# Kernel optimization log

Measured on AMD Instinct MI355X. Metric: run time of the kernel, lower is better.

The kernel has to match this reference:

```python
import jax, jax.numpy as jnp
import numpy as np


def _scinol_new_p(p0, S2, G, eta, M, cond):
    # SCINOL effective-parameter computation (done under no_grad in torch)
    denom = jnp.sqrt(S2 + M * M)
    theta = jnp.clip(G / denom, -1.0, 1.0)
    upd = jnp.where(cond, theta / (2.0 * denom) * eta, 0.0)
    return p0 + jax.lax.stop_gradient(upd)


def _conv(x, w, b):
    y = jax.lax.conv_general_dilated(x, w, window_strides=(1, 1), padding='VALID',
                                     dimension_numbers=('NCHW', 'OIHW', 'NCHW'))
    return y + b[None, :, None, None]


def _maxpool2(x):
    return jax.lax.reduce_window(x, -jnp.inf, jax.lax.max, (1, 1, 2, 2), (1, 1, 2, 2), 'VALID')


def _scinol_conv(x, w0, wS2, wG, weta, wM, b0, bS2, bG, beta):
    # M-update: per-input-channel mean (over batch) of max-abs over H,W
    stat = jax.lax.stop_gradient(jnp.mean(jnp.max(jnp.abs(x), axis=(2, 3)), axis=0))  # (C_in,)
    M = jnp.maximum(stat, wM)  # (C_in,)
    w = _scinol_new_p(w0, wS2, wG, weta, M[None, :, None, None], wG != 0)
    b = _scinol_new_p(b0, bS2, bG, beta, jnp.float32(1.0), bG != 0)
    return _conv(x, w, b)


def _scinol_linear(x, w0, wS2, wG, weta, wM, b0, bS2, bG, beta):
    stat = jax.lax.stop_gradient(jnp.mean(jnp.abs(x), axis=0))  # (in_features,)
    M = jnp.maximum(wM, stat)  # broadcast -> (out, in)
    w = _scinol_new_p(w0, wS2, wG, weta, M, wS2 != 0)
    b = _scinol_new_p(b0, bS2, bG, beta, jnp.float32(1.0), bS2 != 0)
    return x @ w.T + b


def setup_inputs() -> dict:
    key = jax.random.key(0)
    ks = iter(jax.random.split(key, 40))
    f32 = jnp.float32
    d = {}
    d['x'] = jax.random.normal(next(ks), (2048, 1, 28, 28), dtype=f32)
    for pre, wshape, cin in [('c1', (64, 1, 5, 5), 1), ('c2', (64, 64, 5, 5), 64)]:
        d[pre + '_w0'] = jax.random.normal(next(ks), wshape, dtype=f32) * 0.1
        d[pre + '_wS2'] = jax.random.uniform(next(ks), wshape, dtype=f32)
        d[pre + '_wG'] = jax.random.normal(next(ks), wshape, dtype=f32)
        d[pre + '_weta'] = jax.random.uniform(next(ks), wshape, dtype=f32)
        d[pre + '_wM'] = jax.random.uniform(next(ks), (cin,), dtype=f32)
        d[pre + '_b0'] = jax.random.normal(next(ks), (64,), dtype=f32) * 0.1
        d[pre + '_bS2'] = jax.random.uniform(next(ks), (64,), dtype=f32)
        d[pre + '_bG'] = jax.random.normal(next(ks), (64,), dtype=f32)
        d[pre + '_beta'] = jax.random.uniform(next(ks), (64,), dtype=f32)
    d['l_w0'] = jax.random.normal(next(ks), (10, 1024), dtype=f32) * 0.03
    d['l_wS2'] = jax.random.uniform(next(ks), (10, 1024), dtype=f32)
    d['l_wG'] = jax.random.normal(next(ks), (10, 1024), dtype=f32)
    d['l_weta'] = jax.random.uniform(next(ks), (10, 1024), dtype=f32)
    d['l_wM'] = jax.random.uniform(next(ks), (10, 1024), dtype=f32)
    d['l_b0'] = jax.random.normal(next(ks), (10,), dtype=f32) * 0.03
    d['l_bS2'] = jax.random.uniform(next(ks), (10,), dtype=f32)
    d['l_bG'] = jax.random.normal(next(ks), (10,), dtype=f32)
    d['l_beta'] = jax.random.uniform(next(ks), (10,), dtype=f32)
    return d


def reference(x,
              c1_w0, c1_wS2, c1_wG, c1_weta, c1_wM, c1_b0, c1_bS2, c1_bG, c1_beta,
              c2_w0, c2_wS2, c2_wG, c2_weta, c2_wM, c2_b0, c2_bS2, c2_bG, c2_beta,
              l_w0, l_wS2, l_wG, l_weta, l_wM, l_b0, l_bS2, l_bG, l_beta):
    h = _scinol_conv(x, c1_w0, c1_wS2, c1_wG, c1_weta, c1_wM, c1_b0, c1_bS2, c1_bG, c1_beta)
    h = _maxpool2(jax.nn.relu(h))                      # (N,64,12,12)
    h = _scinol_conv(h, c2_w0, c2_wS2, c2_wG, c2_weta, c2_wM, c2_b0, c2_bS2, c2_bG, c2_beta)
    h = _maxpool2(jax.nn.relu(h))                      # (N,64,4,4)
    h = h.reshape(h.shape[0], -1)                      # (N,1024)
    return _scinol_linear(h, l_w0, l_wS2, l_wG, l_weta, l_wM, l_b0, l_bS2, l_bG, l_beta)
```

## Files before the change

### kernel.cpp

```cpp
#include <hip/hip_runtime.h>
#include <hip/hip_bf16.h>

typedef float v4f __attribute__((ext_vector_type(4)));
typedef short v8s __attribute__((ext_vector_type(8)));

#define WS_STAT2   0
#define WS_STATL   64
#define WS_B1      1088
#define WS_B2      1152
#define WS_WL      1216
#define WS_BL      11456
#define WS_IMAX    11520
#define WS_W1F_B   54272
#define WS_WP2_B   62464
#define WS_P1_B    267264
#define WS_P2_B    38016000
#define WS_C1MAX_F 9504000
#define WS_LPART_F 66816

__global__ void k_stat1(const float* __restrict__ x, float* ws) {
    int tid = threadIdx.x;
    int wv = tid >> 6, lane = tid & 63;
    int n = blockIdx.x * 4 + wv;
    const float* p = x + n * 784;
    float m = 0.f;
    for (int i = lane; i < 784; i += 64) m = fmaxf(m, fabsf(p[i]));
#pragma unroll
    for (int off = 32; off; off >>= 1) m = fmaxf(m, __shfl_xor(m, off, 64));
    if (lane == 0) ws[WS_IMAX + n] = m;
}

__global__ void k_prepw1(const float* __restrict__ w0, const float* __restrict__ S2,
                         const float* __restrict__ G, const float* __restrict__ eta,
                         const float* __restrict__ wM,
                         const float* __restrict__ b0, const float* __restrict__ bS2,
                         const float* __restrict__ bG, const float* __restrict__ beta,
                         float* ws) {
    __shared__ float red[256];
    int tid = threadIdx.x;
    float p = 0.f;
    for (int i = tid; i < 2048; i += 256) p += ws[WS_IMAX + i];
    red[tid] = p;
    __syncthreads();
    for (int s = 128; s > 0; s >>= 1) {
        if (tid < s) red[tid] += red[tid + s];
        __syncthreads();
    }
    float M = fmaxf(red[0] * (1.f / 2048.f), wM[0]);

    int i = blockIdx.x * 256 + tid;
    if (i < 4096) {
        int j = i & 7, m16 = (i >> 3) & 15, q = (i >> 7) & 3, ot = i >> 9;
        int tap = q * 8 + j, oc = m16 * 4 + ot;
        float v = 0.f;
        if (tap < 25) {
            int s = oc * 25 + tap;
            float g = G[s];
            float den = sqrtf(S2[s] + M * M);
            float inv = 1.f / den;
            float th = fminf(fmaxf(g * inv, -1.f), 1.f);
            v = w0[s] + ((g != 0.f) ? th * 0.5f * inv * eta[s] : 0.f);
        }
        ((__hip_bfloat16*)((char*)ws + WS_W1F_B))[i] = __float2bfloat16(v);
    } else if (i < 4160) {
        int c = i - 4096;
        float g = bG[c];
        float den = sqrtf(bS2[c] + 1.f);
        float inv = 1.f / den;
        float th = fminf(fmaxf(g * inv, -1.f), 1.f);
        ws[WS_B1 + c] = b0[c] + ((g != 0.f) ? th * 0.5f * inv * beta[c] : 0.f);
    }
}

__global__ void __launch_bounds__(256)
k_conv1(const float* __restrict__ x, float* ws, __hip_bfloat16* __restrict__ pool1) {
    __shared__ __align__(16) float sX[1024];
    __shared__ int sMax[64];
    int n = blockIdx.x, tid = threadIdx.x;
    int wv = tid >> 6, lane = tid & 63;
    int m16 = lane & 15, quad = lane >> 4;

    {
        const float4* src = (const float4*)(x + (size_t)n * 784);
        float4 v = {0.f, 0.f, 0.f, 0.f};
        if (tid < 196) v = src[tid];
        ((float4*)sX)[tid] = v;
    }
    if (tid < 64) sMax[tid] = 0;

    const ushort* wfrag = (const ushort*)((const char*)ws + WS_W1F_B);
    v8s bfr[4];
#pragma unroll
    for (int ot = 0; ot < 4; ++ot)
        bfr[ot] = *(const v8s*)(wfrag + ((ot * 4 + quad) * 16 + m16) * 8);
    float4 bias = *(const float4*)(ws + WS_B1 + m16 * 4);

    int dj[8];
#pragma unroll
    for (int j = 0; j < 8; ++j) {
        int tap = quad * 8 + j;
        int u = (tap * 13) >> 6;
        dj[j] = tap + 23 * u;
    }

    int W0 = wv * 36 + (m16 >> 2);
    int wy = (W0 * 171) >> 11;
    int wx = W0 - wy * 12;
    int coff = 28 * ((m16 >> 1) & 1) + (m16 & 1);

    __syncthreads();

    float vmax[4] = {0.f, 0.f, 0.f, 0.f};
    ushort* op = (ushort*)(pool1 + (size_t)n * 9216);

    float g[8];
    {
        int base = 56 * wy + 2 * wx + coff;
#pragma unroll
        for (int j = 0; j < 8; ++j) g[j] = sX[base + dj[j]];
    }
    for (int mt = 0; mt < 9; ++mt) {
        union { v8s v; ushort us[8]; } ua;
#pragma unroll
        for (int j = 0; j < 8; ++j)
            ua.us[j] = __bfloat16_as_ushort(__float2bfloat16(g[j]));

        wx += 4;
        if (wx >= 12) { wx -= 12; ++wy; }
        if (mt < 8) {
            int nb = 56 * wy + 2 * wx + coff;
#pragma unroll
            for (int j = 0; j < 8; ++j) g[j] = sX[nb + dj[j]];
        }

        v4f z = {0.f, 0.f, 0.f, 0.f};
        v4f acc[4];
#pragma unroll
        for (int ot = 0; ot < 4; ++ot)
            acc[ot] = __builtin_amdgcn_mfma_f32_16x16x32_bf16(ua.v, bfr[ot], z, 0, 0, 0);

        int Wd = (wv * 9 + mt) * 4 + quad;
        ushort4 pk;
#pragma unroll
        for (int ot = 0; ot < 4; ++ot) {
            v4f a = acc[ot];
            float m = fmaxf(fmaxf(a[0], a[1]), fmaxf(a[2], a[3]));
            float pv = fmaxf(m + bias[ot], 0.f);
            vmax[ot] = fmaxf(vmax[ot], pv);
            ((ushort*)&pk)[ot] = __bfloat16_as_ushort(__float2bfloat16(pv));
        }
        *(ushort4*)(op + Wd * 64 + m16 * 4) = pk;
    }

#pragma unroll
    for (int ot = 0; ot < 4; ++ot) {
        float m = vmax[ot];
        m = fmaxf(m, __shfl_xor(m, 16, 64));
        m = fmaxf(m, __shfl_xor(m, 32, 64));
        if (lane < 16) atomicMax(&sMax[lane * 4 + ot], __float_as_int(m));
    }
    __syncthreads();
    if (tid < 64) ws[WS_C1MAX_F + n * 64 + tid] = __int_as_float(sMax[tid]);
}

__global__ void k_stat2red(float* ws) {
    __shared__ float red[256];
    int c = blockIdx.x, t = threadIdx.x;
    float s = 0.f;
    for (int n = t; n < 2048; n += 256) s += ws[WS_C1MAX_F + n * 64 + c];
    red[t] = s;
    __syncthreads();
    for (int k = 128; k > 0; k >>= 1) {
        if (t < k) red[t] += red[t + k];
        __syncthreads();
    }
    if (t == 0) ws[WS_STAT2 + c] = red[0] * (1.f / 2048.f);
}

__global__ void k_prepw2(const float* __restrict__ w0, const float* __restrict__ S2,
                         const float* __restrict__ G, const float* __restrict__ eta,
                         const float* __restrict__ wM,
                         const float* __restrict__ b0, const float* __restrict__ bS2,
                         const float* __restrict__ bG, const float* __restrict__ beta,
                         float* ws, __hip_bfloat16* __restrict__ wp2) {
    int i = blockIdx.x * 256 + threadIdx.x;
    int j = i & 7, m16 = (i >> 3) & 15, quad = (i >> 7) & 3;
    int ot = (i >> 9) & 3, kc = (i >> 11) & 1, uv = i >> 12;
    int oc = ot * 16 + m16, ic = kc * 32 + quad * 8 + j;
    int s = oc * 1600 + ic * 25 + uv;
    float M = fmaxf(ws[WS_STAT2 + ic], wM[ic]);
    float g = G[s];
    float den = sqrtf(S2[s] + M * M);
    float inv = 1.f / den;
    float th = fminf(fmaxf(g * inv, -1.f), 1.f);
    float v = w0[s] + ((g != 0.f) ? th * 0.5f * inv * eta[s] : 0.f);
    wp2[i] = __float2bfloat16(v);
    if (blockIdx.x == 0 && threadIdx.x < 64) {
        int c = threadIdx.x;
        float gb = bG[c];
        float den2 = sqrtf(bS2[c] + 1.f);
        float inv2 = 1.f / den2;
        float th2 = fminf(fmaxf(gb * inv2, -1.f), 1.f);
        ws[WS_B2 + c] = b0[c] + ((gb != 0.f) ? th2 * 0.5f * inv2 * beta[c] : 0.f);
    }
}

#define LOADB(buf, uvi) do {                                                   \
    const ushort* wnext_ = wlane + (uvi) * 4096;                               \
    _Pragma("unroll")                                                          \
    for (int kc_ = 0; kc_ < 2; ++kc_)                                          \
        _Pragma("unroll")                                                      \
        for (int ot_ = 0; ot_ < 4; ++ot_)                                      \
            buf[kc_ * 4 + ot_] = *(const v8s*)(wnext_ + (kc_ * 4 + ot_) * 512);\
} while (0)

#define STEP(buf, uvi) do {                                                    \
    int u_ = (uvi) / 5, v_ = (uvi) % 5;                                        \
    int r0_ = rbase + u_ * 12 + v_;                                            \
    _Pragma("unroll")                                                          \
    for (int kc_ = 0; kc_ < 2; ++kc_) {                                        \
        v8s pA_[4];                                                            \
        _Pragma("unroll")                                                      \
        for (int pt_ = 0; pt_ < 4; ++pt_) {                                    \
            int row_ = r0_ + pt_ * 24;                                         \
            int rs_ = row_ & 7;                                                \
            pA_[pt_] = *(const v8s*)(simg + row_ * 64 +                        \
                                     (((kc_ * 4 + quad) ^ rs_) << 3));         \
        }                                                                      \
        _Pragma("unroll")                                                      \
        for (int pt_ = 0; pt_ < 4; ++pt_)                                      \
            _Pragma("unroll")                                                  \
            for (int ot_ = 0; ot_ < 4; ++ot_)                                  \
                acc[pt_][ot_] = __builtin_amdgcn_mfma_f32_16x16x32_bf16(       \
                    pA_[pt_], buf[kc_ * 4 + ot_], acc[pt_][ot_], 0, 0, 0);     \
    }                                                                          \
} while (0)

__global__ void __launch_bounds__(256, 2)
k_conv2(const ushort* __restrict__ pool1, const ushort* __restrict__ wp2,
        const float* __restrict__ ws, float* __restrict__ pool2) {
    __shared__ __align__(16) ushort sImg[4 * 9216];
    int tid = threadIdx.x;
    int wv = tid >> 6, lane = tid & 63;
    int n0 = blockIdx.x * 4;

    {
        const uint4* src = (const uint4*)(pool1 + (size_t)n0 * 9216);
        uint4* dst = (uint4*)sImg;
#pragma unroll
        for (int img = 0; img < 4; ++img) {
            int b = img * 1152;
#pragma unroll
            for (int i = 0; i < 4; ++i) {
                int c = tid + i * 256;
                int r = c >> 3, col = c & 7;
                dst[b + r * 8 + (col ^ (r & 7))] = src[b + c];
            }
            if (tid < 128) {
                int c = 1024 + tid;
                int r = c >> 3, col = c & 7;
                dst[b + r * 8 + (col ^ (r & 7))] = src[b + c];
            }
        }
    }

    int m16 = lane & 15, quad = lane >> 4;
    int x0 = m16 & 7;
    int yb = m16 >> 3;
    int rbase = yb * 12 + x0;

    v4f acc[4][4];
#pragma unroll
    for (int i = 0; i < 4; ++i)
#pragma unroll
        for (int j = 0; j < 4; ++j) acc[i][j] = (v4f){0.f, 0.f, 0.f, 0.f};

    const ushort* wlane = wp2 + lane * 8;

    v8s b0[8], b1[8];
    LOADB(b0, 0);

    __syncthreads();

    const ushort* simg = sImg + wv * 9216;

#pragma unroll
    for (int t = 0; t < 12; ++t) {
        LOADB(b1, 2 * t + 1);
        STEP(b0, 2 * t);
        LOADB(b0, 2 * t + 2);
        STEP(b1, 2 * t + 1);
    }
    STEP(b0, 24);

    int n = n0 + wv;
    float bv[4];
#pragma unroll
    for (int ot = 0; ot < 4; ++ot) bv[ot] = ws[WS_B2 + ot * 16 + m16];
    float* outp = pool2 + (size_t)n * 1024;
#pragma unroll
    for (int pt = 0; pt < 4; ++pt)
#pragma unroll
        for (int ot = 0; ot < 4; ++ot) {
            v4f a = acc[pt][ot];
            float m01 = fmaxf(a[0], a[1]);
            float m23 = fmaxf(a[2], a[3]);
            m01 = fmaxf(m01, __shfl_xor(m01, 32, 64));
            m23 = fmaxf(m23, __shfl_xor(m23, 32, 64));
            if (lane < 32) {
                int oc = ot * 16 + m16;
                int f = oc * 16 + pt * 4 + (quad & 1) * 2;
                outp[f] = fmaxf(m01 + bv[ot], 0.f);
                outp[f + 1] = fmaxf(m23 + bv[ot], 0.f);
            }
        }
}

__global__ void k_statl(const float* __restrict__ pool2, float* ws) {
    int b = blockIdx.x, tid = threadIdx.x;
    float4 s = {0.f, 0.f, 0.f, 0.f};
    for (int im = 0; im < 32; ++im) {
        float4 v = ((const float4*)(pool2 + (size_t)(b * 32 + im) * 1024))[tid];
        s.x += v.x; s.y += v.y; s.z += v.z; s.w += v.w;
    }
    ((float4*)(ws + WS_LPART_F + b * 1024))[tid] = s;
}

__global__ void k_prepwl(const float* __restrict__ w0, const float* __restrict__ S2,
                         const float* __restrict__ G, const float* __restrict__ eta,
                         const float* __restrict__ wM,
                         const float* __restrict__ b0, const float* __restrict__ bS2,
                         const float* __restrict__ bG, const float* __restrict__ beta,
                         float* ws) {
    int i = blockIdx.x * 256 + threadIdx.x;
    if (i < 10240) {
        int f = i & 1023;
        float s = 0.f;
#pragma unroll
        for (int b = 0; b < 64; ++b) s += ws[WS_LPART_F + b * 1024 + f];
        float stat = s * (1.f / 2048.f);
        float M = fmaxf(wM[i], stat);
        float s2 = S2[i];
        float den = sqrtf(s2 + M * M);
        float inv = 1.f / den;
        float th = fminf(fmaxf(G[i] * inv, -1.f), 1.f);
        ws[WS_WL + i] = w0[i] + ((s2 != 0.f) ? th * 0.5f * inv * eta[i] : 0.f);
    } else if (i < 10250) {
        int c = i - 10240;
        float s2 = bS2[c];
        float den = sqrtf(s2 + 1.f);
        float inv = 1.f / den;
        float th = fminf(fmaxf(bG[c] * inv, -1.f), 1.f);
        ws[WS_BL + c] = b0[c] + ((s2 != 0.f) ? th * 0.5f * inv * beta[c] : 0.f);
    }
}

__global__ void k_linear(const float* __restrict__ pool2, const float* __restrict__ ws,
                         float* __restrict__ out) {
    int tid = threadIdx.x;
    int wv = tid >> 6, lane = tid & 63;
    int n = blockIdx.x * 4 + wv;
    const float* hp = pool2 + (size_t)n * 1024;
    float h[16];
#pragma unroll
    for (int j = 0; j < 16; ++j) h[j] = hp[j * 64 + lane];
    for (int oc = 0; oc < 10; ++oc) {
        const float* wp = ws + WS_WL + oc * 1024;
        float d = 0.f;
#pragma unroll
        for (int j = 0; j < 16; ++j) d = fmaf(h[j], wp[j * 64 + lane], d);
#pragma unroll
        for (int off = 32; off; off >>= 1) d += __shfl_xor(d, off, 64);
        if (lane == 0) out[n * 10 + oc] = d + ws[WS_BL + oc];
    }
}

extern "C" void kernel_launch(void* const* d_in, const int* in_sizes, int n_in,
                              void* d_out, int out_size, void* d_ws, size_t ws_size,
                              hipStream_t stream) {
    const float* x = (const float*)d_in[0];
    float* ws = (float*)d_ws;
    __hip_bfloat16* wp2 = (__hip_bfloat16*)((char*)d_ws + WS_WP2_B);
    __hip_bfloat16* p1 = (__hip_bfloat16*)((char*)d_ws + WS_P1_B);
    float* p2 = (float*)((char*)d_ws + WS_P2_B);
    float* out = (float*)d_out;

    k_stat1<<<512, 256, 0, stream>>>(x, ws);
    k_prepw1<<<17, 256, 0, stream>>>(
        (const float*)d_in[1], (const float*)d_in[2], (const float*)d_in[3],
        (const float*)d_in[4], (const float*)d_in[5], (const float*)d_in[6],
        (const float*)d_in[7], (const float*)d_in[8], (const float*)d_in[9], ws);
    k_conv1<<<2048, 256, 0, stream>>>(x, ws, p1);
    k_stat2red<<<64, 256, 0, stream>>>(ws);
    k_prepw2<<<400, 256, 0, stream>>>(
        (const float*)d_in[10], (const float*)d_in[11], (const float*)d_in[12],
        (const float*)d_in[13], (const float*)d_in[14], (const float*)d_in[15],
        (const float*)d_in[16], (const float*)d_in[17], (const float*)d_in[18], ws, wp2);
    k_conv2<<<512, 256, 0, stream>>>((const ushort*)p1, (const ushort*)wp2, ws, p2);
    k_statl<<<64, 256, 0, stream>>>(p2, ws);
    k_prepwl<<<41, 256, 0, stream>>>(
        (const float*)d_in[19], (const float*)d_in[20], (const float*)d_in[21],
        (const float*)d_in[22], (const float*)d_in[23], (const float*)d_in[24],
        (const float*)d_in[25], (const float*)d_in[26], (const float*)d_in[27], ws);
    k_linear<<<512, 256, 0, stream>>>(p2, ws, out);
}
```

Baseline: 200.9 us.

## Stage conv2 weights through LDS with double-buffered A fragments

In conv2, each wave used to fetch weight fragments straight from global memory. Now the block cooperatively loads each weight slice into a shared LDS buffer, prefetches the next slices into registers, and separates the steps with barriers. Image fragments are double-buffered in registers so the next tap loads while the current MFMAs run. Conv1 now converts its input tile to bf16 once when filling LDS rather than on every use. The linear-layer statistic reduction uses twice as many blocks. The conv2 change cuts redundant global weight traffic but adds block-wide barriers and brings LDS use close to the per-CU limit at two blocks per CU.

After: 196.1 us. -2.4%, faster.

```diff
diff --git a/kernel.cpp b/kernel.cpp
--- a/kernel.cpp
+++ b/kernel.cpp
@@ -74,7 +74,7 @@
 
 __global__ void __launch_bounds__(256)
 k_conv1(const float* __restrict__ x, float* ws, __hip_bfloat16* __restrict__ pool1) {
-    __shared__ __align__(16) float sX[1024];
+    __shared__ __align__(16) ushort sXh[1024];
     __shared__ int sMax[64];
     int n = blockIdx.x, tid = threadIdx.x;
     int wv = tid >> 6, lane = tid & 63;
@@ -84,7 +84,12 @@
         const float4* src = (const float4*)(x + (size_t)n * 784);
         float4 v = {0.f, 0.f, 0.f, 0.f};
         if (tid < 196) v = src[tid];
-        ((float4*)sX)[tid] = v;
+        ushort4 h;
+        h.x = __bfloat16_as_ushort(__float2bfloat16(v.x));
+        h.y = __bfloat16_as_ushort(__float2bfloat16(v.y));
+        h.z = __bfloat16_as_ushort(__float2bfloat16(v.z));
+        h.w = __bfloat16_as_ushort(__float2bfloat16(v.w));
+        ((ushort4*)sXh)[tid] = h;
     }
     if (tid < 64) sMax[tid] = 0;
 
@@ -113,24 +118,23 @@
     float vmax[4] = {0.f, 0.f, 0.f, 0.f};
     ushort* op = (ushort*)(pool1 + (size_t)n * 9216);
 
-    float g[8];
+    ushort g[8];
     {
         int base = 56 * wy + 2 * wx + coff;
 #pragma unroll
-        for (int j = 0; j < 8; ++j) g[j] = sX[base + dj[j]];
+        for (int j = 0; j < 8; ++j) g[j] = sXh[base + dj[j]];
     }
     for (int mt = 0; mt < 9; ++mt) {
         union { v8s v; ushort us[8]; } ua;
 #pragma unroll
-        for (int j = 0; j < 8; ++j)
-            ua.us[j] = __bfloat16_as_ushort(__float2bfloat16(g[j]));
+        for (int j = 0; j < 8; ++j) ua.us[j] = g[j];
 
         wx += 4;
         if (wx >= 12) { wx -= 12; ++wy; }
         if (mt < 8) {
             int nb = 56 * wy + 2 * wx + coff;
 #pragma unroll
-            for (int j = 0; j < 8; ++j) g[j] = sX[nb + dj[j]];
+            for (int j = 0; j < 8; ++j) g[j] = sXh[nb + dj[j]];
         }
 
         v4f z = {0.f, 0.f, 0.f, 0.f};
@@ -205,41 +209,51 @@
     }
 }
 
-#define LOADB(buf, uvi) do {                                                   \
-    const ushort* wnext_ = wlane + (uvi) * 4096;                               \
-    _Pragma("unroll")                                                          \
-    for (int kc_ = 0; kc_ < 2; ++kc_)                                          \
-        _Pragma("unroll")                                                      \
-        for (int ot_ = 0; ot_ < 4; ++ot_)                                      \
-            buf[kc_ * 4 + ot_] = *(const v8s*)(wnext_ + (kc_ * 4 + ot_) * 512);\
-} while (0)
-
-#define STEP(buf, uvi) do {                                                    \
+
+#define LOADA(Aset, uvi) do {                                                  \
     int u_ = (uvi) / 5, v_ = (uvi) % 5;                                        \
     int r0_ = rbase + u_ * 12 + v_;                                            \
     _Pragma("unroll")                                                          \
-    for (int kc_ = 0; kc_ < 2; ++kc_) {                                        \
-        v8s pA_[4];                                                            \
+    for (int kc_ = 0; kc_ < 2; ++kc_)                                          \
         _Pragma("unroll")                                                      \
         for (int pt_ = 0; pt_ < 4; ++pt_) {                                    \
             int row_ = r0_ + pt_ * 24;                                         \
             int rs_ = row_ & 7;                                                \
-            pA_[pt_] = *(const v8s*)(simg + row_ * 64 +                        \
+            Aset[kc_ * 4 + pt_] = *(const v8s*)(simg + row_ * 64 +             \
                                      (((kc_ * 4 + quad) ^ rs_) << 3));         \
         }                                                                      \
+} while (0)
+
+#define LOADPB() do {                                                          \
+    _Pragma("unroll")                                                          \
+    for (int q_ = 0; q_ < 8; ++q_)                                             \
+        pB[q_] = *(const v8s*)(sB + q_ * 512 + lane * 8);                      \
+} while (0)
+
+#define DOMFMA(Aset) do {                                                      \
+    _Pragma("unroll")                                                          \
+    for (int kc_ = 0; kc_ < 2; ++kc_)                                          \
         _Pragma("unroll")                                                      \
         for (int pt_ = 0; pt_ < 4; ++pt_)                                      \
             _Pragma("unroll")                                                  \
             for (int ot_ = 0; ot_ < 4; ++ot_)                                  \
                 acc[pt_][ot_] = __builtin_amdgcn_mfma_f32_16x16x32_bf16(       \
-                    pA_[pt_], buf[kc_ * 4 + ot_], acc[pt_][ot_], 0, 0, 0);     \
-    }                                                                          \
+                    Aset[kc_ * 4 + pt_], pB[kc_ * 4 + ot_], acc[pt_][ot_],     \
+                    0, 0, 0);                                                  \
+} while (0)
+
+#define BAR_LDS() do {                                                         \
+    asm volatile("s_waitcnt lgkmcnt(0)" ::: "memory");                         \
+    __builtin_amdgcn_sched_barrier(0);                                         \
+    __builtin_amdgcn_s_barrier();                                              \
+    __builtin_amdgcn_sched_barrier(0);                                         \
 } while (0)
 
 __global__ void __launch_bounds__(256, 2)
 k_conv2(const ushort* __restrict__ pool1, const ushort* __restrict__ wp2,
         const float* __restrict__ ws, float* __restrict__ pool2) {
     __shared__ __align__(16) ushort sImg[4 * 9216];
+    __shared__ __align__(16) ushort sB[4096];
     int tid = threadIdx.x;
     int wv = tid >> 6, lane = tid & 63;
     int n0 = blockIdx.x * 4;
@@ -275,23 +289,51 @@
 #pragma unroll
         for (int j = 0; j < 4; ++j) acc[i][j] = (v4f){0.f, 0.f, 0.f, 0.f};
 
-    const ushort* wlane = wp2 + lane * 8;
-
-    v8s b0[8], b1[8];
-    LOADB(b0, 0);
+    const uint4* bsrc = (const uint4*)wp2;
+    uint4 g00 = bsrc[tid], g01 = bsrc[256 + tid];
 
     __syncthreads();
 
+    ((uint4*)sB)[tid] = g00;
+    ((uint4*)sB)[256 + tid] = g01;
+    uint4 ga0 = bsrc[512 + tid],  ga1 = bsrc[768 + tid];
+    uint4 gb0 = bsrc[1024 + tid], gb1 = bsrc[1280 + tid];
+
     const ushort* simg = sImg + wv * 9216;
-
-#pragma unroll
+    v8s Aa[8], Ab[8], pB[8];
+    LOADA(Aa, 0);
+
+    BAR_LDS();
+
+#pragma unroll 1
     for (int t = 0; t < 12; ++t) {
-        LOADB(b1, 2 * t + 1);
-        STEP(b0, 2 * t);
-        LOADB(b0, 2 * t + 2);
-        STEP(b1, 2 * t + 1);
-    }
-    STEP(b0, 24);
+        int e = 2 * t;
+        LOADPB();
+        LOADA(Ab, e + 1);
+        DOMFMA(Aa);
+        BAR_LDS();
+        ((uint4*)sB)[tid] = ga0;
+        ((uint4*)sB)[256 + tid] = ga1;
+        if (e + 3 < 25) {
+            const uint4* nb = bsrc + (e + 3) * 512;
+            ga0 = nb[tid]; ga1 = nb[256 + tid];
+        }
+        BAR_LDS();
+
+        LOADPB();
+        LOADA(Aa, e + 2);
+        DOMFMA(Ab);
+        BAR_LDS();
+        ((uint4*)sB)[tid] = gb0;
+        ((uint4*)sB)[256 + tid] = gb1;
+        if (e + 4 < 25) {
+            const uint4* nb = bsrc + (e + 4) * 512;
+            gb0 = nb[tid]; gb1 = nb[256 + tid];
+        }
+        BAR_LDS();
+    }
+    LOADPB();
+    DOMFMA(Aa);
 
     int n = n0 + wv;
     float bv[4];
@@ -319,8 +361,8 @@
 __global__ void k_statl(const float* __restrict__ pool2, float* ws) {
     int b = blockIdx.x, tid = threadIdx.x;
     float4 s = {0.f, 0.f, 0.f, 0.f};
-    for (int im = 0; im < 32; ++im) {
-        float4 v = ((const float4*)(pool2 + (size_t)(b * 32 + im) * 1024))[tid];
+    for (int im = 0; im < 16; ++im) {
+        float4 v = ((const float4*)(pool2 + (size_t)(b * 16 + im) * 1024))[tid];
         s.x += v.x; s.y += v.y; s.z += v.z; s.w += v.w;
     }
     ((float4*)(ws + WS_LPART_F + b * 1024))[tid] = s;
@@ -336,8 +378,8 @@
     if (i < 10240) {
         int f = i & 1023;
         float s = 0.f;
-#pragma unroll
-        for (int b = 0; b < 64; ++b) s += ws[WS_LPART_F + b * 1024 + f];
+#pragma unroll 8
+        for (int b = 0; b < 128; ++b) s += ws[WS_LPART_F + b * 1024 + f];
         float stat = s * (1.f / 2048.f);
         float M = fmaxf(wM[i], stat);
         float s2 = S2[i];
@@ -397,7 +439,7 @@
         (const float*)d_in[13], (const float*)d_in[14], (const float*)d_in[15],
         (const float*)d_in[16], (const float*)d_in[17], (const float*)d_in[18], ws, wp2);
     k_conv2<<<512, 256, 0, stream>>>((const ushort*)p1, (const ushort*)wp2, ws, p2);
-    k_statl<<<64, 256, 0, stream>>>(p2, ws);
+    k_statl<<<128, 256, 0, stream>>>(p2, ws);
     k_prepwl<<<41, 256, 0, stream>>>(
         (const float*)d_in[19], (const float*)d_in[20], (const float*)d_in[21],
         (const float*)d_in[22], (const float*)d_in[23], (const float*)d_in[24],
```
